# Kernel optimization log

Measured on AMD Instinct MI355X. Metric: run time of the kernel, lower is better.

The kernel has to match this reference:

```python
import jax, jax.numpy as jnp
import numpy as np

N_NODES = 20000
N_EDGES = 320000
IN_CH = 512
HID = 128
HEADS = 4
OUT_CH = 256
NEG_SLOPE = 0.2


def _gat_layer(x, edge_index, W, a_src, a_dst, bias, heads, out_ch, concat):
    """PyG GATConv (add_self_loops=True, eval mode: no dropout).
    x: [N, F_in], edge_index: [2, E] (row 0 = src, row 1 = dst).
    Returns (out, alpha) with alpha: [E+N, heads].
    """
    N = x.shape[0]
    h = (x @ W).reshape(N, heads, out_ch)                      # [N, H, C]
    loops = jnp.arange(N, dtype=edge_index.dtype)
    src = jnp.concatenate([edge_index[0], loops])
    dst = jnp.concatenate([edge_index[1], loops])
    a_s = jnp.einsum('nhc,hc->nh', h, a_src)                   # [N, H]
    a_d = jnp.einsum('nhc,hc->nh', h, a_dst)
    e = a_s[src] + a_d[dst]                                    # [E', H]
    e = jnp.where(e > 0, e, NEG_SLOPE * e)                     # LeakyReLU
    # segment softmax over incoming edges of each dst node
    emax = jax.ops.segment_max(e, dst, num_segments=N)
    ex = jnp.exp(e - emax[dst])
    denom = jax.ops.segment_sum(ex, dst, num_segments=N)
    alpha = ex / denom[dst]                                    # [E', H]
    msg = alpha[:, :, None] * h[src]                           # [E', H, C]
    out = jax.ops.segment_sum(msg, dst, num_segments=N)        # [N, H, C]
    out = out.reshape(N, heads * out_ch) if concat else out.mean(axis=1)
    return out + bias, alpha


def setup_inputs() -> dict:
    key = jax.random.key(0)
    ks = jax.random.split(key, 10)
    s = 0.05
    x = jax.random.normal(ks[0], (N_NODES, IN_CH), dtype=jnp.float32)
    edge_index = jax.random.randint(ks[1], (2, N_EDGES), 0, N_NODES, dtype=jnp.int32)
    W1 = jax.random.normal(ks[2], (IN_CH, HEADS * HID), dtype=jnp.float32) * s
    a_src1 = jax.random.normal(ks[3], (HEADS, HID), dtype=jnp.float32) * s
    a_dst1 = jax.random.normal(ks[4], (HEADS, HID), dtype=jnp.float32) * s
    b1 = jnp.zeros((HEADS * HID,), dtype=jnp.float32)
    W2 = jax.random.normal(ks[5], (HEADS * HID, OUT_CH), dtype=jnp.float32) * s
    a_src2 = jax.random.normal(ks[6], (1, OUT_CH), dtype=jnp.float32) * s
    a_dst2 = jax.random.normal(ks[7], (1, OUT_CH), dtype=jnp.float32) * s
    b2 = jnp.zeros((OUT_CH,), dtype=jnp.float32)
    return {"x": x, "edge_index": edge_index, "W1": W1, "a_src1": a_src1,
            "a_dst1": a_dst1, "b1": b1, "W2": W2, "a_src2": a_src2,
            "a_dst2": a_dst2, "b2": b2}


def reference(x, edge_index, W1, a_src1, a_dst1, b1, W2, a_src2, a_dst2, b2):
    h, alpha1 = _gat_layer(x, edge_index, W1, a_src1, a_dst1, b1, HEADS, HID, True)
    h = jax.nn.elu(h)
    # dropout inactive in eval mode
    out, alpha2 = _gat_layer(h, edge_index, W2, a_src2, a_dst2, b2, 1, OUT_CH, False)
    return out, alpha1, alpha2
```

## Files before the change

kernel.cpp:

```cpp
#include <hip/hip_runtime.h>
#include <hip/hip_bf16.h>
#include <cstdint>


#define NNODES 20000
#define NEDGES 320000
#define ETOT   340000
#define F1     512
#define F2     256
#define HEADS  4

typedef __bf16 bf16;
typedef __attribute__((ext_vector_type(8))) __bf16 bf16x8;
typedef __attribute__((ext_vector_type(4))) float f32x4;

__device__ __forceinline__ float bflo(unsigned p) { return __uint_as_float(p << 16); }
__device__ __forceinline__ float bfhi(unsigned p) { return __uint_as_float(p & 0xffff0000u); }

__device__ __forceinline__ void gload_lds16(const void* g, void* l) {
    __builtin_amdgcn_global_load_lds(
        (const __attribute__((address_space(1))) void*)g,
        (__attribute__((address_space(3))) void*)l, 16, 0, 0);
}

__global__ void deg_count(const int* __restrict__ ei, int* __restrict__ deg) {
    int e = blockIdx.x * blockDim.x + threadIdx.x;
    if (e >= ETOT) return;
    int dst = (e < NEDGES) ? ei[NEDGES + e] : (e - NEDGES);
    atomicAdd(&deg[dst], 1);
}

__global__ void scan_deg(const int* __restrict__ deg, int* __restrict__ offs,
                         int* __restrict__ cur) {
    __shared__ int sums[1024];
    const int t = threadIdx.x;
    const int PER = 20;
    int base = t * PER;
    int local[PER];
    int run = 0;
#pragma unroll
    for (int j = 0; j < PER; j++) {
        int i = base + j;
        int v = (i < NNODES) ? deg[i] : 0;
        local[j] = run;
        run += v;
    }
    sums[t] = run;
    __syncthreads();
    for (int o = 1; o < 1024; o <<= 1) {
        int v = (t >= o) ? sums[t - o] : 0;
        __syncthreads();
        sums[t] += v;
        __syncthreads();
    }
    int texcl = (t == 0) ? 0 : sums[t - 1];
#pragma unroll
    for (int j = 0; j < PER; j++) {
        int i = base + j;
        if (i < NNODES) {
            int e = texcl + local[j];
            cur[i] = e;
            offs[i] = e;
        }
    }
    if (t == 1023) offs[NNODES] = sums[1023];
}

__global__ void fill_csr(const int* __restrict__ ei, int* __restrict__ cur,
                         int* __restrict__ csr_src, int* __restrict__ csr_eid) {
    int e = blockIdx.x * blockDim.x + threadIdx.x;
    if (e >= ETOT) return;
    int src, dst;
    if (e < NEDGES) { src = ei[e]; dst = ei[NEDGES + e]; }
    else            { src = dst = e - NEDGES; }
    int p = atomicAdd(&cur[dst], 1);
    csr_src[p] = src;
    csr_eid[p] = e;
}

__global__ void swizzle_w(const float* __restrict__ W, bf16* __restrict__ Wh,
                          bf16* __restrict__ Wl, int K, int N) {
    int idx = blockIdx.x * blockDim.x + threadIdx.x;
    int total = (K * N) >> 3;
    if (idx >= total) return;
    int lane = idx & 63;
    int tile = idx >> 6;
    int NT = N >> 4;
    int kt = tile / NT, nt = tile - kt * NT;
    int krow = kt * 32 + (lane >> 4) * 8;
    int col  = nt * 16 + (lane & 15);
    union { bf16 b[8]; uint4 u; } hi, lo;
#pragma unroll
    for (int j = 0; j < 8; j++) {
        float w = W[(size_t)(krow + j) * N + col];
        bf16 h = (bf16)w;
        hi.b[j] = h;
        lo.b[j] = (bf16)(w - (float)h);
    }
    *(uint4*)(Wh + (size_t)idx * 8) = hi.u;
    *(uint4*)(Wl + (size_t)idx * 8) = lo.u;
}

__global__ void split_f32(const float* __restrict__ X, bf16* __restrict__ Xh,
                          bf16* __restrict__ Xl, int total8) {
    int i = blockIdx.x * blockDim.x + threadIdx.x;
    if (i >= total8) return;
    float v[8];
    *(float4*)(v)     = *(const float4*)(X + (size_t)i * 8);
    *(float4*)(v + 4) = *(const float4*)(X + (size_t)i * 8 + 4);
    union { bf16 b[8]; uint4 u; } h, l;
#pragma unroll
    for (int j = 0; j < 8; j++) {
        bf16 hh = (bf16)v[j];
        h.b[j] = hh;
        l.b[j] = (bf16)(v[j] - (float)hh);
    }
    *(uint4*)(Xh + (size_t)i * 8) = h.u;
    *(uint4*)(Xl + (size_t)i * 8) = l.u;
}

template <int K, int N>
__global__ __launch_bounds__(256) void gemm_fused(const bf16* __restrict__ Ah,
                                                  const bf16* __restrict__ Al,
                                                  const bf16* __restrict__ Bh,
                                                  const bf16* __restrict__ Bl,
                                                  bf16* __restrict__ Cb,
                                                  const float* __restrict__ asrc,
                                                  const float* __restrict__ adst,
                                                  float* __restrict__ as_out,
                                                  float* __restrict__ ad_out, int M) {
    __shared__ __align__(16) char smem[2][8192];
    const int lane = threadIdx.x & 63;
    const int wave = threadIdx.x >> 6;
    const int row_base = blockIdx.x * 128 + wave * 32;
    const int colt0 = blockIdx.y * 4;
    constexpr int NT = N / 16;
    constexpr int NKT = K / 32;

    const char* hbase = (const char*)Bh + (size_t)colt0 * 1024;
    const char* lbase = (const char*)Bl + (size_t)colt0 * 1024;
    auto stage = [&](int kt, int buf) {
        size_t kb = (size_t)kt * NT * 1024;
#pragma unroll
        for (int q = 0; q < 2; q++) {
            int off = wave * 2048 + q * 1024;
            const char* src = (off < 4096) ? (hbase + kb + off)
                                           : (lbase + kb + (off - 4096));
            gload_lds16(src + lane * 16, &smem[buf][off]);
        }
    };

    int arow0 = row_base + (lane & 15);
    int arow1 = arow0 + 16;
    if (arow0 >= M) arow0 = M - 1;
    if (arow1 >= M) arow1 = M - 1;
    const int ko = (lane >> 4) * 8;
    const bf16* pah0 = Ah + (size_t)arow0 * K + ko;
    const bf16* pal0 = Al + (size_t)arow0 * K + ko;
    const bf16* pah1 = Ah + (size_t)arow1 * K + ko;
    const bf16* pal1 = Al + (size_t)arow1 * K + ko;

    f32x4 acc0[4] = {}, acc1[4] = {};
    bf16x8 ah0 = *(const bf16x8*)pah0;
    bf16x8 al0 = *(const bf16x8*)pal0;
    bf16x8 ah1 = *(const bf16x8*)pah1;
    bf16x8 al1 = *(const bf16x8*)pal1;

    auto body = [&](const char* bb) {
#pragma unroll
        for (int c = 0; c < 4; c++) {
            bf16x8 bh = *(const bf16x8*)(bb + c * 1024 + lane * 16);
            bf16x8 bl = *(const bf16x8*)(bb + 4096 + c * 1024 + lane * 16);
            acc0[c] = __builtin_amdgcn_mfma_f32_16x16x32_bf16(ah0, bh, acc0[c], 0, 0, 0);
            acc1[c] = __builtin_amdgcn_mfma_f32_16x16x32_bf16(ah1, bh, acc1[c], 0, 0, 0);
            acc0[c] = __builtin_amdgcn_mfma_f32_16x16x32_bf16(ah0, bl, acc0[c], 0, 0, 0);
            acc1[c] = __builtin_amdgcn_mfma_f32_16x16x32_bf16(ah1, bl, acc1[c], 0, 0, 0);
            acc0[c] = __builtin_amdgcn_mfma_f32_16x16x32_bf16(al0, bh, acc0[c], 0, 0, 0);
            acc1[c] = __builtin_amdgcn_mfma_f32_16x16x32_bf16(al1, bh, acc1[c], 0, 0, 0);
        }
    };

    stage(0, 0);
    __syncthreads();
    for (int kt = 0; kt < NKT - 1; ++kt) {
        stage(kt + 1, (kt + 1) & 1);
        bf16x8 nah0 = *(const bf16x8*)(pah0 + (kt + 1) * 32);
        bf16x8 nal0 = *(const bf16x8*)(pal0 + (kt + 1) * 32);
        bf16x8 nah1 = *(const bf16x8*)(pah1 + (kt + 1) * 32);
        bf16x8 nal1 = *(const bf16x8*)(pal1 + (kt + 1) * 32);
        body(smem[kt & 1]);
        __syncthreads();
        ah0 = nah0; al0 = nal0; ah1 = nah1; al1 = nal1;
    }
    body(smem[(NKT - 1) & 1]);

    const int crow0 = row_base + (lane >> 4) * 4;
    const int col15 = lane & 15;
#pragma unroll
    for (int c = 0; c < 4; c++)
#pragma unroll
        for (int r = 0; r < 4; r++) {
            int r0 = crow0 + r, r1 = r0 + 16;
            int cc = (colt0 + c) * 16 + col15;
            if (r0 < M) Cb[(size_t)r0 * N + cc] = (bf16)acc0[c][r];
            if (r1 < M) Cb[(size_t)r1 * N + cc] = (bf16)acc1[c][r];
        }

    float ss0[4] = {}, sd0[4] = {}, ss1[4] = {}, sd1[4] = {};
#pragma unroll
    for (int c = 0; c < 4; c++) {
        int cw = blockIdx.y * 64 + c * 16 + col15;
        float was = asrc[cw];
        float wad = adst[cw];
#pragma unroll
        for (int r = 0; r < 4; r++) {
            ss0[r] += acc0[c][r] * was; sd0[r] += acc0[c][r] * wad;
            ss1[r] += acc1[c][r] * was; sd1[r] += acc1[c][r] * wad;
        }
    }
#pragma unroll
    for (int o = 1; o < 16; o <<= 1)
#pragma unroll
        for (int r = 0; r < 4; r++) {
            ss0[r] += __shfl_xor(ss0[r], o); sd0[r] += __shfl_xor(sd0[r], o);
            ss1[r] += __shfl_xor(ss1[r], o); sd1[r] += __shfl_xor(sd1[r], o);
        }
    if (col15 == 0) {
        constexpr int HS = (N == 512) ? 4 : 1;
        const int head = (N == 512) ? (blockIdx.y >> 1) : 0;
#pragma unroll
        for (int r = 0; r < 4; r++) {
            int r0 = crow0 + r, r1 = r0 + 16;
            if (r0 < M) {
                atomicAdd(&as_out[r0 * HS + head], ss0[r]);
                atomicAdd(&ad_out[r0 * HS + head], sd0[r]);
            }
            if (r1 < M) {
                atomicAdd(&as_out[r1 * HS + head], ss1[r]);
                atomicAdd(&ad_out[r1 * HS + head], sd1[r]);
            }
        }
    }
}

__global__ __launch_bounds__(64) void agg1(const bf16* __restrict__ h1b,
                                           const float* __restrict__ as1,
                                           const float* __restrict__ ad1,
                                           const int* __restrict__ offs,
                                           const int* __restrict__ csr_src,
                                           const int* __restrict__ csr_eid,
                                           const float* __restrict__ b1,
                                           float* __restrict__ alpha1,
                                           bf16* __restrict__ h1eh,
                                           bf16* __restrict__ h1el) {
    const int n = blockIdx.x;
    const int lane = threadIdx.x;
    const int beg = offs[n];
    const int deg = offs[n + 1] - beg;

    __shared__ int   s_src[64];
    __shared__ float s_al[64][4];

    float4 ad4 = *(const float4*)(ad1 + n * 4);
    const float adn[4] = {ad4.x, ad4.y, ad4.z, ad4.w};

    float v0[4];
    int s0 = 0, e0 = 0;
    float mx[4] = {-3e38f, -3e38f, -3e38f, -3e38f};
    for (int idx = lane; idx < deg; idx += 64) {
        int s = csr_src[beg + idx];
        float4 a4 = *(const float4*)(as1 + s * 4);
        float v[4] = {a4.x + adn[0], a4.y + adn[1], a4.z + adn[2], a4.w + adn[3]};
#pragma unroll
        for (int h = 0; h < 4; h++) {
            v[h] = v[h] > 0.f ? v[h] : 0.2f * v[h];
            mx[h] = fmaxf(mx[h], v[h]);
        }
        if (idx == lane) {
            s0 = s; e0 = csr_eid[beg + idx];
#pragma unroll
            for (int h = 0; h < 4; h++) v0[h] = v[h];
        }
    }
#pragma unroll
    for (int o = 1; o < 64; o <<= 1)
#pragma unroll
        for (int h = 0; h < 4; h++) mx[h] = fmaxf(mx[h], __shfl_xor(mx[h], o));

    float ex0[4] = {0.f, 0.f, 0.f, 0.f};
    float ls[4] = {0.f, 0.f, 0.f, 0.f};
    if (lane < deg) {
#pragma unroll
        for (int h = 0; h < 4; h++) { ex0[h] = __expf(v0[h] - mx[h]); ls[h] = ex0[h]; }
    }
    for (int idx = lane + 64; idx < deg; idx += 64) {
        int s = csr_src[beg + idx];
        float4 a4 = *(const float4*)(as1 + s * 4);
        float v[4] = {a4.x + adn[0], a4.y + adn[1], a4.z + adn[2], a4.w + adn[3]};
#pragma unroll
        for (int h = 0; h < 4; h++) {
            v[h] = v[h] > 0.f ? v[h] : 0.2f * v[h];
            ls[h] += __expf(v[h] - mx[h]);
        }
    }
#pragma unroll
    for (int o = 1; o < 64; o <<= 1)
#pragma unroll
        for (int h = 0; h < 4; h++) ls[h] += __shfl_xor(ls[h], o);
    float rden[4];
#pragma unroll
    for (int h = 0; h < 4; h++) rden[h] = 1.f / ls[h];

    float acc[8] = {};
    const int myh = lane >> 4;
    for (int base = 0; base < deg; base += 64) {
        int idx = base + lane;
        if (idx < deg) {
            int s, e;
            float al[4];
            if (base == 0) {
                s = s0; e = e0;
#pragma unroll
                for (int h = 0; h < 4; h++) al[h] = ex0[h] * rden[h];
            } else {
                s = csr_src[beg + idx];
                e = csr_eid[beg + idx];
                float4 a4 = *(const float4*)(as1 + s * 4);
                float v[4] = {a4.x + adn[0], a4.y + adn[1], a4.z + adn[2], a4.w + adn[3]};
#pragma unroll
                for (int h = 0; h < 4; h++) {
                    v[h] = v[h] > 0.f ? v[h] : 0.2f * v[h];
                    al[h] = __expf(v[h] - mx[h]) * rden[h];
                }
            }
            s_src[lane] = s;
#pragma unroll
            for (int h = 0; h < 4; h++) s_al[lane][h] = al[h];
            *(float4*)(alpha1 + (size_t)e * 4) = make_float4(al[0], al[1], al[2], al[3]);
        }
        __syncthreads();
        int cnt = min(64, deg - base);
        for (int i = 0; i < cnt; i++) {
            int s = s_src[i];
            float a = s_al[i][myh];
            uint4 p = *(const uint4*)(h1b + (size_t)s * F1 + lane * 8);
            acc[0] += a * bflo(p.x); acc[1] += a * bfhi(p.x);
            acc[2] += a * bflo(p.y); acc[3] += a * bfhi(p.y);
            acc[4] += a * bflo(p.z); acc[5] += a * bfhi(p.z);
            acc[6] += a * bflo(p.w); acc[7] += a * bfhi(p.w);
        }
        __syncthreads();
    }
    const int c8 = lane * 8;
    float bv[8];
    *(float4*)(bv)     = *(const float4*)(b1 + c8);
    *(float4*)(bv + 4) = *(const float4*)(b1 + c8 + 4);
    union { bf16 b[8]; uint4 u; } hh, ll;
#pragma unroll
    for (int j = 0; j < 8; j++) {
        float t = acc[j] + bv[j];
        float o = t > 0.f ? t : expm1f(t);
        bf16 hb = (bf16)o;
        hh.b[j] = hb;
        ll.b[j] = (bf16)(o - (float)hb);
    }
    *(uint4*)(h1eh + (size_t)n * F1 + c8) = hh.u;
    *(uint4*)(h1el + (size_t)n * F1 + c8) = ll.u;
}

__global__ __launch_bounds__(64) void agg2(const bf16* __restrict__ h2b,
                                           const float* __restrict__ as2,
                                           const float* __restrict__ ad2,
                                           const int* __restrict__ offs,
                                           const int* __restrict__ csr_src,
                                           const int* __restrict__ csr_eid,
                                           const float* __restrict__ b2,
                                           float* __restrict__ alpha2,
                                           float* __restrict__ out) {
    const int n = blockIdx.x;
    const int lane = threadIdx.x;
    const int beg = offs[n];
    const int deg = offs[n + 1] - beg;

    __shared__ int   s_src[64];
    __shared__ float s_al[64];

    const float adn = ad2[n];

    float v0 = 0.f;
    int s0 = 0, e0 = 0;
    float mx = -3e38f;
    for (int idx = lane; idx < deg; idx += 64) {
        int s = csr_src[beg + idx];
        float v = as2[s] + adn;
        v = v > 0.f ? v : 0.2f * v;
        mx = fmaxf(mx, v);
        if (idx == lane) { s0 = s; e0 = csr_eid[beg + idx]; v0 = v; }
    }
#pragma unroll
    for (int o = 1; o < 64; o <<= 1) mx = fmaxf(mx, __shfl_xor(mx, o));

    float ex0 = 0.f, ls = 0.f;
    if (lane < deg) { ex0 = __expf(v0 - mx); ls = ex0; }
    for (int idx = lane + 64; idx < deg; idx += 64) {
        int s = csr_src[beg + idx];
        float v = as2[s] + adn;
        v = v > 0.f ? v : 0.2f * v;
        ls += __expf(v - mx);
    }
#pragma unroll
    for (int o = 1; o < 64; o <<= 1) ls += __shfl_xor(ls, o);
    float rden = 1.f / ls;

    float acc[4] = {};
    for (int base = 0; base < deg; base += 64) {
        int idx = base + lane;
        if (idx < deg) {
            int s, e;
            float a;
            if (base == 0) { s = s0; e = e0; a = ex0 * rden; }
            else {
                s = csr_src[beg + idx];
                e = csr_eid[beg + idx];
                float v = as2[s] + adn;
                v = v > 0.f ? v : 0.2f * v;
                a = __expf(v - mx) * rden;
            }
            s_src[lane] = s;
            s_al[lane] = a;
            alpha2[e] = a;
        }
        __syncthreads();
        int cnt = min(64, deg - base);
        for (int i = 0; i < cnt; i++) {
            int s = s_src[i];
            float a = s_al[i];
            uint2 p = *(const uint2*)(h2b + (size_t)s * F2 + lane * 4);
            acc[0] += a * bflo(p.x); acc[1] += a * bfhi(p.x);
            acc[2] += a * bflo(p.y); acc[3] += a * bfhi(p.y);
        }
        __syncthreads();
    }
    const int c4 = lane * 4;
    float4 bv = *(const float4*)(b2 + c4);
    *(float4*)(out + (size_t)n * F2 + c4) =
        make_float4(acc[0] + bv.x, acc[1] + bv.y, acc[2] + bv.z, acc[3] + bv.w);
}

extern "C" void kernel_launch(void* const* d_in, const int* in_sizes, int n_in,
                              void* d_out, int out_size, void* d_ws, size_t ws_size,
                              hipStream_t stream) {
    const float* x      = (const float*)d_in[0];
    const int*   ei     = (const int*)d_in[1];
    const float* W1     = (const float*)d_in[2];
    const float* a_src1 = (const float*)d_in[3];
    const float* a_dst1 = (const float*)d_in[4];
    const float* b1     = (const float*)d_in[5];
    const float* W2     = (const float*)d_in[6];
    const float* a_src2 = (const float*)d_in[7];
    const float* a_dst2 = (const float*)d_in[8];
    const float* b2     = (const float*)d_in[9];

    char* ws = (char*)d_ws;
    size_t off = 0;
    auto alloc = [&](size_t bytes) -> char* {
        char* p = ws + off;
        off += (bytes + 255) & ~(size_t)255;
        return p;
    };
    bf16*  h1b  = (bf16*) alloc((size_t)NNODES * F1 * 2);
    bf16*  h2b  = (bf16*) alloc((size_t)NNODES * F2 * 2);
    bf16*  h1eh = (bf16*) alloc((size_t)NNODES * F1 * 2);
    bf16*  h1el = (bf16*) alloc((size_t)NNODES * F1 * 2);
    bf16*  Xh   = (bf16*) alloc((size_t)NNODES * F1 * 2);
    bf16*  Xl   = (bf16*) alloc((size_t)NNODES * F1 * 2);
    float* as1  = (float*)alloc((size_t)NNODES * 4 * 4);
    float* ad1  = (float*)alloc((size_t)NNODES * 4 * 4);
    float* as2  = (float*)alloc((size_t)NNODES * 4);
    float* ad2  = (float*)alloc((size_t)NNODES * 4);
    bf16*  W1h  = (bf16*) alloc((size_t)512 * 512 * 2);
    bf16*  W1l  = (bf16*) alloc((size_t)512 * 512 * 2);
    bf16*  W2h  = (bf16*) alloc((size_t)512 * 256 * 2);
    bf16*  W2l  = (bf16*) alloc((size_t)512 * 256 * 2);
    int*   deg  = (int*)  alloc((size_t)NNODES * 4);
    int*   offs = (int*)  alloc((size_t)(NNODES + 1) * 4);
    int*   cur  = (int*)  alloc((size_t)NNODES * 4);
    int*   csrS = (int*)  alloc((size_t)ETOT * 4);
    int*   csrE = (int*)  alloc((size_t)ETOT * 4);

    float* out2   = (float*)d_out;
    float* alpha1 = out2 + (size_t)NNODES * F2;
    float* alpha2 = alpha1 + (size_t)ETOT * HEADS;

    hipMemsetAsync(deg, 0, (size_t)NNODES * 4, stream);
    hipMemsetAsync(as1, 0, (size_t)NNODES * 4 * 4, stream);
    hipMemsetAsync(ad1, 0, (size_t)NNODES * 4 * 4, stream);
    hipMemsetAsync(as2, 0, (size_t)NNODES * 4, stream);
    hipMemsetAsync(ad2, 0, (size_t)NNODES * 4, stream);
    deg_count<<<(ETOT + 255) / 256, 256, 0, stream>>>(ei, deg);
    scan_deg<<<1, 1024, 0, stream>>>(deg, offs, cur);
    fill_csr<<<(ETOT + 255) / 256, 256, 0, stream>>>(ei, cur, csrS, csrE);

    swizzle_w<<<(512 * 512 / 8 + 255) / 256, 256, 0, stream>>>(W1, W1h, W1l, 512, 512);
    swizzle_w<<<(512 * 256 / 8 + 255) / 256, 256, 0, stream>>>(W2, W2h, W2l, 512, 256);
    split_f32<<<(NNODES * F1 / 8 + 255) / 256, 256, 0, stream>>>(
        x, Xh, Xl, NNODES * F1 / 8);

    gemm_fused<512, 512><<<dim3(157, 8), 256, 0, stream>>>(
        Xh, Xl, W1h, W1l, h1b, a_src1, a_dst1, as1, ad1, NNODES);
    agg1<<<NNODES, 64, 0, stream>>>(h1b, as1, ad1, offs, csrS, csrE, b1, alpha1,
                                    h1eh, h1el);

    gemm_fused<512, 256><<<dim3(157, 4), 256, 0, stream>>>(
        h1eh, h1el, W2h, W2l, h2b, a_src2, a_dst2, as2, ad2, NNODES);
    agg2<<<NNODES, 64, 0, stream>>>(h2b, as2, ad2, offs, csrS, csrE, b2, alpha2, out2);
}
```

Baseline: 370.7 us.

## Widen GEMM column tile to 128, swizzle block order, drop layer-1 atomics

The GEMM now computes 128 output columns per block instead of 64, which doubles the LDS stage and the accumulator count and halves the re-reads of A tiles. A 1D grid with a grouped block-index remap keeps blocks that share A rows running close together, aiming for better L2 reuse. Because one block now covers a full head in layer 1, the attention-score partial sums are written directly, so the atomics and two memsets go away. The cost is higher register pressure from 64 accumulator floats per lane plus the extra A/B fragments, which may lower occupancy.

```diff
diff --git a/kernel.cpp b/kernel.cpp
--- a/kernel.cpp
+++ b/kernel.cpp
@@ -119,7 +119,7 @@
     *(uint4*)(Xl + (size_t)i * 8) = l.u;
 }
 
-template <int K, int N>
+template <int K, int N, int NYB>
 __global__ __launch_bounds__(256) void gemm_fused(const bf16* __restrict__ Ah,
                                                   const bf16* __restrict__ Al,
                                                   const bf16* __restrict__ Bh,
@@ -129,23 +129,42 @@
                                                   const float* __restrict__ adst,
                                                   float* __restrict__ as_out,
                                                   float* __restrict__ ad_out, int M) {
-    __shared__ __align__(16) char smem[2][8192];
+    __shared__ __align__(16) char smem[2][16384];
     const int lane = threadIdx.x & 63;
     const int wave = threadIdx.x >> 6;
-    const int row_base = blockIdx.x * 128 + wave * 32;
-    const int colt0 = blockIdx.y * 4;
     constexpr int NT = N / 16;
     constexpr int NKT = K / 32;
+    constexpr int CH = 8 * NYB;
+
+    const int nb = gridDim.x;
+    const int full = (nb / CH) * CH;
+    int bx, by;
+    {
+        int id = blockIdx.x;
+        if (id < full) {
+            int chunk = id / CH, pos = id % CH;
+            bx = chunk * 8 + (pos & 7);
+            by = pos >> 3;
+        } else {
+            int r = id - full;
+            int x0 = full / NYB;
+            int remx = nb / NYB - x0;
+            bx = x0 + r % remx;
+            by = r / remx;
+        }
+    }
+    const int row_base = bx * 128 + wave * 32;
+    const int colt0 = by * 8;
 
     const char* hbase = (const char*)Bh + (size_t)colt0 * 1024;
     const char* lbase = (const char*)Bl + (size_t)colt0 * 1024;
     auto stage = [&](int kt, int buf) {
         size_t kb = (size_t)kt * NT * 1024;
 #pragma unroll
-        for (int q = 0; q < 2; q++) {
-            int off = wave * 2048 + q * 1024;
-            const char* src = (off < 4096) ? (hbase + kb + off)
-                                           : (lbase + kb + (off - 4096));
+        for (int q = 0; q < 4; q++) {
+            int off = wave * 4096 + q * 1024;
+            const char* src = (off < 8192) ? (hbase + kb + off)
+                                           : (lbase + kb + (off - 8192));
             gload_lds16(src + lane * 16, &smem[buf][off]);
         }
     };
@@ -160,7 +179,7 @@
     const bf16* pah1 = Ah + (size_t)arow1 * K + ko;
     const bf16* pal1 = Al + (size_t)arow1 * K + ko;
 
-    f32x4 acc0[4] = {}, acc1[4] = {};
+    f32x4 acc0[8] = {}, acc1[8] = {};
     bf16x8 ah0 = *(const bf16x8*)pah0;
     bf16x8 al0 = *(const bf16x8*)pal0;
     bf16x8 ah1 = *(const bf16x8*)pah1;
@@ -168,9 +187,9 @@
 
     auto body = [&](const char* bb) {
 #pragma unroll
-        for (int c = 0; c < 4; c++) {
+        for (int c = 0; c < 8; c++) {
             bf16x8 bh = *(const bf16x8*)(bb + c * 1024 + lane * 16);
-            bf16x8 bl = *(const bf16x8*)(bb + 4096 + c * 1024 + lane * 16);
+            bf16x8 bl = *(const bf16x8*)(bb + 8192 + c * 1024 + lane * 16);
             acc0[c] = __builtin_amdgcn_mfma_f32_16x16x32_bf16(ah0, bh, acc0[c], 0, 0, 0);
             acc1[c] = __builtin_amdgcn_mfma_f32_16x16x32_bf16(ah1, bh, acc1[c], 0, 0, 0);
             acc0[c] = __builtin_amdgcn_mfma_f32_16x16x32_bf16(ah0, bl, acc0[c], 0, 0, 0);
@@ -197,7 +216,7 @@
     const int crow0 = row_base + (lane >> 4) * 4;
     const int col15 = lane & 15;
 #pragma unroll
-    for (int c = 0; c < 4; c++)
+    for (int c = 0; c < 8; c++)
 #pragma unroll
         for (int r = 0; r < 4; r++) {
             int r0 = crow0 + r, r1 = r0 + 16;
@@ -208,8 +227,8 @@
 
     float ss0[4] = {}, sd0[4] = {}, ss1[4] = {}, sd1[4] = {};
 #pragma unroll
-    for (int c = 0; c < 4; c++) {
-        int cw = blockIdx.y * 64 + c * 16 + col15;
+    for (int c = 0; c < 8; c++) {
+        int cw = by * 128 + c * 16 + col15;
         float was = asrc[cw];
         float wad = adst[cw];
 #pragma unroll
@@ -226,18 +245,19 @@
             ss1[r] += __shfl_xor(ss1[r], o); sd1[r] += __shfl_xor(sd1[r], o);
         }
     if (col15 == 0) {
-        constexpr int HS = (N == 512) ? 4 : 1;
-        const int head = (N == 512) ? (blockIdx.y >> 1) : 0;
-#pragma unroll
-        for (int r = 0; r < 4; r++) {
-            int r0 = crow0 + r, r1 = r0 + 16;
-            if (r0 < M) {
-                atomicAdd(&as_out[r0 * HS + head], ss0[r]);
-                atomicAdd(&ad_out[r0 * HS + head], sd0[r]);
+        if constexpr (N == 512) {
+#pragma unroll
+            for (int r = 0; r < 4; r++) {
+                int r0 = crow0 + r, r1 = r0 + 16;
+                if (r0 < M) { as_out[r0 * 4 + by] = ss0[r]; ad_out[r0 * 4 + by] = sd0[r]; }
+                if (r1 < M) { as_out[r1 * 4 + by] = ss1[r]; ad_out[r1 * 4 + by] = sd1[r]; }
             }
-            if (r1 < M) {
-                atomicAdd(&as_out[r1 * HS + head], ss1[r]);
-                atomicAdd(&ad_out[r1 * HS + head], sd1[r]);
+        } else {
+#pragma unroll
+            for (int r = 0; r < 4; r++) {
+                int r0 = crow0 + r, r1 = r0 + 16;
+                if (r0 < M) { atomicAdd(&as_out[r0], ss0[r]); atomicAdd(&ad_out[r0], sd0[r]); }
+                if (r1 < M) { atomicAdd(&as_out[r1], ss1[r]); atomicAdd(&ad_out[r1], sd1[r]); }
             }
         }
     }
@@ -493,8 +513,6 @@
     float* alpha2 = alpha1 + (size_t)ETOT * HEADS;
 
     hipMemsetAsync(deg, 0, (size_t)NNODES * 4, stream);
-    hipMemsetAsync(as1, 0, (size_t)NNODES * 4 * 4, stream);
-    hipMemsetAsync(ad1, 0, (size_t)NNODES * 4 * 4, stream);
     hipMemsetAsync(as2, 0, (size_t)NNODES * 4, stream);
     hipMemsetAsync(ad2, 0, (size_t)NNODES * 4, stream);
     deg_count<<<(ETOT + 255) / 256, 256, 0, stream>>>(ei, deg);
@@ -506,12 +524,12 @@
     split_f32<<<(NNODES * F1 / 8 + 255) / 256, 256, 0, stream>>>(
         x, Xh, Xl, NNODES * F1 / 8);
 
-    gemm_fused<512, 512><<<dim3(157, 8), 256, 0, stream>>>(
+    gemm_fused<512, 512, 4><<<157 * 4, 256, 0, stream>>>(
         Xh, Xl, W1h, W1l, h1b, a_src1, a_dst1, as1, ad1, NNODES);
     agg1<<<NNODES, 64, 0, stream>>>(h1b, as1, ad1, offs, csrS, csrE, b1, alpha1,
                                     h1eh, h1el);
 
-    gemm_fused<512, 256><<<dim3(157, 4), 256, 0, stream>>>(
+    gemm_fused<512, 256, 2><<<157 * 2, 256, 0, stream>>>(
         h1eh, h1el, W2h, W2l, h2b, a_src2, a_dst2, as2, ad2, NNODES);
     agg2<<<NNODES, 64, 0, stream>>>(h2b, as2, ad2, offs, csrS, csrE, b2, alpha2, out2);
 }
```

Result: faster. 346.0 us (-6.6%).
